# Optimization experiments

Measured on AMD Instinct MI355X. Metric: run time of the kernel, lower is better.

Reference implementation:

```python
import jax, jax.numpy as jnp
import numpy as np

# DH-SFNN: 2 dendritic LIF layers (denri, no tanh, reset-by-subtraction) + leaky readout integrator.
GAMMA = 0.5   # surrogate gradient scale
LENS = 0.5    # surrogate gradient width
VTH = 1.0     # spike threshold
DT = 1.0

@jax.custom_vjp
def spike_fn(x):
    # Heaviside forward, Gaussian surrogate backward (act_fun_adp)
    return (x > 0.0).astype(x.dtype)

def _spike_fwd(x):
    return spike_fn(x), x

def _spike_bwd(x, g):
    sg = GAMMA * jnp.exp(-x * x / (2.0 * LENS * LENS)) / (jnp.sqrt(2.0 * jnp.pi) * LENS)
    return (g * sg,)

spike_fn.defvjp(_spike_fwd, _spike_bwd)

B, T, IN, H, O, K = 256, 250, 700, 256, 20, 4  # batch, time, in_dim, hidden, out_dim, branch
WARMUP = 10


def _branch_mask(rng, out_dim, in_dim, k):
    # Each neuron's k branches see a disjoint random partition of the inputs.
    m = np.zeros((out_dim * k, in_dim), np.float32)
    step = in_dim // k
    for i in range(out_dim):
        perm = rng.permutation(in_dim)
        for j in range(k):
            m[i * k + j, perm[j * step:(j + 1) * step]] = 1.0
    return m


def setup_inputs() -> dict:
    key = jax.random.key(0)
    ks = jax.random.split(key, 12)
    rng = np.random.default_rng(0)
    s1 = 1.0 / np.sqrt(IN)
    s2 = 1.0 / np.sqrt(H)
    # branch-masked dense weights (apply_mask() already baked in)
    W1 = jax.random.uniform(ks[0], (H * K, IN), minval=-s1, maxval=s1) * jnp.asarray(_branch_mask(rng, H, IN, K))
    b1 = jax.random.uniform(ks[1], (H * K,), minval=-s1, maxval=s1)
    tau_n1 = jax.random.uniform(ks[2], (H, K), minval=2.0, maxval=6.0)
    tau_m1 = jax.random.uniform(ks[3], (H,), minval=0.0, maxval=4.0)
    W2 = jax.random.uniform(ks[4], (H * K, H), minval=-s2, maxval=s2) * jnp.asarray(_branch_mask(rng, H, H, K))
    b2 = jax.random.uniform(ks[5], (H * K,), minval=-s2, maxval=s2)
    tau_n2 = jax.random.uniform(ks[6], (H, K), minval=2.0, maxval=6.0)
    tau_m2 = jax.random.uniform(ks[7], (H,), minval=0.0, maxval=4.0)
    Wr = jax.random.uniform(ks[8], (O, H), minval=-s2, maxval=s2)
    br = jax.random.uniform(ks[9], (O,), minval=-s2, maxval=s2)
    tau_mr = jax.random.uniform(ks[10], (O,), minval=0.0, maxval=4.0)
    # sparse binary spike train input (SHD-like)
    x = (jax.random.uniform(ks[11], (B, T, IN)) < 0.1).astype(jnp.float32)
    return dict(x=x, W1=W1, b1=b1, tau_n1=tau_n1, tau_m1=tau_m1,
                W2=W2, b2=b2, tau_n2=tau_n2, tau_m2=tau_m2,
                Wr=Wr, br=br, tau_mr=tau_mr, warmup=WARMUP)


def reference(x, W1, b1, tau_n1, tau_m1, W2, b2, tau_n2, tau_m2, Wr, br, tau_mr, warmup):
    Bb, Tt, _ = x.shape
    beta1 = jax.nn.sigmoid(tau_n1)   # [H,K] dendritic decay
    alpha1 = jax.nn.sigmoid(tau_m1)  # [H]   soma decay
    beta2 = jax.nn.sigmoid(tau_n2)
    alpha2 = jax.nn.sigmoid(tau_m2)
    alphar = jax.nn.sigmoid(tau_mr)  # [O]

    def dense_branch(inp, W, b):
        return (inp @ W.T + b).reshape(inp.shape[0], -1, K)  # [B,H,K]

    def step(carry, xt):
        d1, m1, s1, d2, m2, s2, mr, acc, t = carry
        # layer 1: dendritic filtering then LIF with soft reset
        d1 = beta1 * d1 + (1.0 - beta1) * dense_branch(xt, W1, b1)
        m1 = m1 * alpha1 + (1.0 - alpha1) * DT * d1.sum(-1) - VTH * s1
        s1 = spike_fn(m1 - VTH)
        # layer 2
        d2 = beta2 * d2 + (1.0 - beta2) * dense_branch(s1, W2, b2)
        m2 = m2 * alpha2 + (1.0 - alpha2) * DT * d2.sum(-1) - VTH * s2
        s2 = spike_fn(m2 - VTH)
        # leaky readout integrator
        mr = mr * alphar + (1.0 - alphar) * (s2 @ Wr.T + br)
        acc = acc + jnp.where(t >= warmup, mr, jnp.zeros_like(mr))
        return (d1, m1, s1, d2, m2, s2, mr, acc, t + 1), None

    z = lambda *s: jnp.zeros(s, x.dtype)
    carry0 = (z(Bb, H, K), z(Bb, H), z(Bb, H),
              z(Bb, H, K), z(Bb, H), z(Bb, H),
              z(Bb, O), z(Bb, O), jnp.int32(0))
    carry, _ = jax.lax.scan(step, carry0, jnp.moveaxis(x, 1, 0))
    acc = carry[7]
    return acc / (Tt - warmup)  # readout_mode == 'mean'
```

## Files before the change

### kernel.cpp

```cpp
#include <hip/hip_runtime.h>
#include <hip/hip_bf16.h>

typedef unsigned short us16;
typedef unsigned int u32;
typedef unsigned long long ull;

#define B_   256
#define T_   250
#define IN_  700
#define KP_  704
#define H_   256
#define O_   20
#define HK_  1024
#define NPAIR_ (B_ * T_)
#define LDP_ 40
#define CP_  136
#define CVT_ROWB_ ((NPAIR_ + HK_) / 4)
#define CVT_W2B_  64

typedef __attribute__((ext_vector_type(8))) short short8;
typedef __attribute__((ext_vector_type(4))) float f32x4;

__device__ __forceinline__ float bfbits(unsigned int lo16) {
    union { unsigned int i; float f; } v; v.i = lo16 << 16; return v.f;
}
__device__ __forceinline__ float bflo(unsigned int u) {
    union { unsigned int i; float f; } v; v.i = u << 16; return v.f;
}
__device__ __forceinline__ float bfhi(unsigned int u) {
    union { unsigned int i; float f; } v; v.i = u & 0xffff0000u; return v.f;
}
__device__ __forceinline__ us16 f2bfu(float f) {
    __hip_bfloat16 h = __float2bfloat16(f);
    union { __hip_bfloat16 h; us16 u; } c; c.h = h; return c.u;
}
__device__ __forceinline__ float sigm(float x) { return 1.0f / (1.0f + expf(-x)); }
__device__ __forceinline__ int rfl(int v) { return __builtin_amdgcn_readfirstlane(v); }

__device__ __forceinline__ bool detect_bf16(const us16* __restrict__ taun) {
    int ok = 0;
#pragma unroll
    for (int i = 0; i < 8; i += 2) ok += ((taun[i] >> 8) == 0x40) ? 1 : 0;
    return ok == 4;
}
__device__ __forceinline__ float ldany(const void* __restrict__ p, long i, bool isb) {
    return isb ? bfbits(((const us16*)p)[i]) : ((const float*)p)[i];
}

__device__ __forceinline__ void async_cp16(const us16* g, us16* l) {
    __builtin_amdgcn_global_load_lds(
        (const __attribute__((address_space(1))) u32*)g,
        (__attribute__((address_space(3))) u32*)l, 16, 0, 0);
}

__global__ __launch_bounds__(256) void cvt_rows2(
    const void* __restrict__ xin, const void* __restrict__ w1in,
    const void* __restrict__ w2in,
    us16* __restrict__ xout, us16* __restrict__ w1out,
    us16* __restrict__ w2t,
    const us16* __restrict__ taun) {
    const bool isb = detect_bf16(taun);

    if (blockIdx.x >= CVT_ROWB_) {
        const int base = (blockIdx.x - CVT_ROWB_) * 256 + threadIdx.x;
        for (int e = base; e < H_ * HK_; e += CVT_W2B_ * 256) {
            const int c = e >> 10, n = e & (HK_ - 1);
            w2t[e] = f2bfu(ldany(w2in, (long)n * H_ + c, isb));
        }
        return;
    }

    const int r = blockIdx.x * 4 + (threadIdx.x >> 6);
    const int l = threadIdx.x & 63;
    const void* in; us16* out; long ibase, obase;
    if (r < NPAIR_) {
        in = xin;  out = xout;  ibase = (long)r * IN_; obase = (long)r * KP_;
    } else {
        const int r2 = r - NPAIR_;
        if (r2 >= HK_) return;
        in = w1in; out = w1out; ibase = (long)r2 * IN_; obase = (long)r2 * KP_;
    }
    for (int c = l; c < 88; c += 64) {
        uint4 o;
        if (c < 87) {
            if (isb) {
                uint2 lo = *(const uint2*)((const us16*)in + ibase + 8 * c);
                uint2 hi = *(const uint2*)((const us16*)in + ibase + 8 * c + 4);
                o.x = lo.x; o.y = lo.y; o.z = hi.x; o.w = hi.y;
            } else {
                float4 f0 = *(const float4*)((const float*)in + ibase + 8 * c);
                float4 f1 = *(const float4*)((const float*)in + ibase + 8 * c + 4);
                o.x = (u32)f2bfu(f0.x) | ((u32)f2bfu(f0.y) << 16);
                o.y = (u32)f2bfu(f0.z) | ((u32)f2bfu(f0.w) << 16);
                o.z = (u32)f2bfu(f1.x) | ((u32)f2bfu(f1.y) << 16);
                o.w = (u32)f2bfu(f1.z) | ((u32)f2bfu(f1.w) << 16);
            }
        } else {
            o.z = 0u; o.w = 0u;
            if (isb) {
                uint2 lo = *(const uint2*)((const us16*)in + ibase + 696);
                o.x = lo.x; o.y = lo.y;
            } else {
                float4 f0 = *(const float4*)((const float*)in + ibase + 696);
                o.x = (u32)f2bfu(f0.x) | ((u32)f2bfu(f0.y) << 16);
                o.y = (u32)f2bfu(f0.z) | ((u32)f2bfu(f0.w) << 16);
            }
        }
        *(uint4*)(out + obase + 8 * c) = o;
    }
}

__global__ void transpose_to_bf16(const void* __restrict__ in, us16* __restrict__ out,
                                  int R, int C, const us16* __restrict__ taun) {
    const bool isb = detect_bf16(taun);
    __shared__ us16 tile[32][33];
    int c0 = blockIdx.x * 32, r0 = blockIdx.y * 32;
    int tx = threadIdx.x, ty = threadIdx.y;
#pragma unroll
    for (int j = 0; j < 32; j += 8) {
        int r = r0 + ty + j, c = c0 + tx;
        if (r < R && c < C) tile[ty + j][tx] = f2bfu(ldany(in, (long)r * C + c, isb));
    }
    __syncthreads();
#pragma unroll
    for (int j = 0; j < 32; j += 8) {
        int c = c0 + ty + j, r = r0 + tx;
        if (c < C && r < R) out[(long)c * R + r] = tile[tx][ty + j];
    }
}

__global__ __launch_bounds__(256) void gemm_bf(
    const us16* __restrict__ Xb, const us16* __restrict__ W1b,
    us16* __restrict__ Apre)
{
    __shared__ __align__(16) us16 smem[32768];

    const int L  = blockIdx.x;
    const int mt = (L & 7) + ((L >> 6) << 3);
    const int nt = (L >> 3) & 7;
    if (mt >= NPAIR_ / 128) return;
    const int m0 = mt * 128, n0 = nt * 128;

    const int tid  = threadIdx.x;
    const int lane = tid & 63;
    const int w    = tid >> 6;
    const int wr   = w >> 1, wc = w & 1;
    const int l16  = lane & 15, quad = lane >> 4;

    const int rr    = lane >> 3;
    const int ccsw  = ((lane & 7) ^ rr) * 8;
    const us16* xg[4]; const us16* wg[4];
    int asl[4], bsl[4];
#pragma unroll
    for (int i = 0; i < 4; ++i) {
        const int blkrow = (w * 4 + i) * 8;
        xg[i]  = Xb  + (long)(m0 + blkrow + rr) * KP_ + ccsw;
        wg[i]  = W1b + (long)(n0 + blkrow + rr) * KP_ + ccsw;
        asl[i] = (w * 4 + i) * 512;
        bsl[i] = 8192 + (w * 4 + i) * 512;
    }

    f32x4 acc[4][4];
#pragma unroll
    for (int i = 0; i < 4; ++i)
#pragma unroll
        for (int j = 0; j < 4; ++j) acc[i][j] = (f32x4){0.f, 0.f, 0.f, 0.f};

    const int sw = l16 & 7;
    int aoff0[4], aoff1[4], boff0[4], boff1[4];
#pragma unroll
    for (int i = 0; i < 4; ++i) {
        const int ar = wr * 64 + i * 16 + l16;
        const int br = wc * 64 + i * 16 + l16;
        aoff0[i] = ar * 64 + ((quad ^ sw) << 3);
        aoff1[i] = ar * 64 + (((quad + 4) ^ sw) << 3);
        boff0[i] = 8192 + br * 64 + ((quad ^ sw) << 3);
        boff1[i] = 8192 + br * 64 + (((quad + 4) ^ sw) << 3);
    }

#pragma unroll
    for (int i = 0; i < 4; ++i) async_cp16(xg[i], smem + asl[i]);
#pragma unroll
    for (int i = 0; i < 4; ++i) async_cp16(wg[i], smem + bsl[i]);
    __syncthreads();

    for (int s = 0; s < 11; ++s) {
        const int cur = (s & 1) * 16384;
        const int nxt = 16384 - cur;
        if (s + 1 < 11) {
            const int kb = (s + 1) * 64;
#pragma unroll
            for (int i = 0; i < 4; ++i) async_cp16(xg[i] + kb, smem + nxt + asl[i]);
#pragma unroll
            for (int i = 0; i < 4; ++i) async_cp16(wg[i] + kb, smem + nxt + bsl[i]);
        }

        short8 af[4][2], bfv[4][2];
#pragma unroll
        for (int i = 0; i < 4; ++i) {
            af[i][0]  = *(const short8*)(smem + cur + aoff0[i]);
            af[i][1]  = *(const short8*)(smem + cur + aoff1[i]);
            bfv[i][0] = *(const short8*)(smem + cur + boff0[i]);
            bfv[i][1] = *(const short8*)(smem + cur + boff1[i]);
        }
#pragma unroll
        for (int h = 0; h < 2; ++h)
#pragma unroll
            for (int i = 0; i < 4; ++i)
#pragma unroll
                for (int j = 0; j < 4; ++j)
                    acc[i][j] = __builtin_amdgcn_mfma_f32_16x16x32_bf16(
                        af[i][h], bfv[j][h], acc[i][j], 0, 0, 0);

        __syncthreads();
    }

#pragma unroll
    for (int i = 0; i < 4; ++i)
#pragma unroll
        for (int j = 0; j < 4; ++j)
#pragma unroll
            for (int r = 0; r < 4; ++r)
                smem[(wr * 64 + i * 16 + quad * 4 + r) * CP_ +
                     (wc * 64 + j * 16 + l16)] = f2bfu(acc[i][j][r]);
    __syncthreads();
    {
        const int c8 = (lane & 15) * 8;
#pragma unroll
        for (int r2 = 0; r2 < 8; ++r2) {
            const int row = w * 32 + r2 * 4 + (lane >> 4);
            const uint4 v = *(const uint4*)(smem + row * CP_ + c8);
            *(uint4*)(Apre + (long)(m0 + row) * HK_ + n0 + c8) = v;
        }
    }
}

__device__ void wave_recur(
    const us16* __restrict__ Apre,
    const void* __restrict__ b1,  const void* __restrict__ tau_n1,
    const void* __restrict__ tau_m1,
    const void* __restrict__ b2,  const void* __restrict__ tau_n2,
    const void* __restrict__ tau_m2,
    const void* __restrict__ Wr,  const void* __restrict__ br,
    const void* __restrict__ tau_mr,
    const us16* __restrict__ W2T,
    int wu, bool isb, int b, int lane,
    void* __restrict__ out)
{
    float be1[16], cb1[16], be2[16], cb2[16], d1[16], d2[16];
#pragma unroll
    for (int e = 0; e < 16; ++e) {
        const long gi = (long)lane * 16 + e;
        const float t1 = sigm(ldany(tau_n1, gi, isb));
        be1[e] = t1; cb1[e] = (1.f - t1) * ldany(b1, gi, isb);
        const float t2 = sigm(ldany(tau_n2, gi, isb));
        be2[e] = t2; cb2[e] = (1.f - t2) * ldany(b2, gi, isb);
        d1[e] = 0.f; d2[e] = 0.f;
    }
    float al1[4], al2[4], m1[4], s1[4], m2[4], s2[4];
#pragma unroll
    for (int j = 0; j < 4; ++j) {
        al1[j] = sigm(ldany(tau_m1, lane * 4 + j, isb));
        al2[j] = sigm(ldany(tau_m2, lane * 4 + j, isb));
        m1[j] = 0.f; s1[j] = 0.f; m2[j] = 0.f; s2[j] = 0.f;
    }
    float alr = 0.f, brv = 0.f;
    if (lane < O_) { alr = sigm(ldany(tau_mr, lane, isb)); brv = ldany(br, lane, isb); }
    float mrv = 0.f, accO = 0.f;

    const us16* ap = Apre + (long)b * T_ * HK_ + lane * 16;

    auto wstep = [&](int t, uint4 lo, uint4 hi) {
        float a[16];
        a[0]=bflo(lo.x);  a[1]=bfhi(lo.x);  a[2]=bflo(lo.y);  a[3]=bfhi(lo.y);
        a[4]=bflo(lo.z);  a[5]=bfhi(lo.z);  a[6]=bflo(lo.w);  a[7]=bfhi(lo.w);
        a[8]=bflo(hi.x);  a[9]=bfhi(hi.x);  a[10]=bflo(hi.y); a[11]=bfhi(hi.y);
        a[12]=bflo(hi.z); a[13]=bfhi(hi.z); a[14]=bflo(hi.w); a[15]=bfhi(hi.w);
#pragma unroll
        for (int e = 0; e < 16; ++e)
            d1[e] = be1[e] * d1[e] + cb1[e] + (1.f - be1[e]) * a[e];
        unsigned long long bal1[4];
#pragma unroll
        for (int j = 0; j < 4; ++j) {
            const float s = (d1[j*4+0] + d1[j*4+1]) + (d1[j*4+2] + d1[j*4+3]);
            m1[j] = m1[j] * al1[j] + (1.f - al1[j]) * s - s1[j];
            s1[j] = (m1[j] > 1.0f) ? 1.f : 0.f;
            bal1[j] = __ballot(s1[j] > 0.f);
        }
        if ((bal1[0] | bal1[1] | bal1[2] | bal1[3]) != 0ull) {
            float g[16];
#pragma unroll
            for (int e = 0; e < 16; ++e) g[e] = 0.f;
            for (int j2 = 0; j2 < 4; ++j2) {
                unsigned long long mm = bal1[j2];
                while (mm) {
                    const int i = __ffsll(mm) - 1; mm &= mm - 1;
                    const us16* wv = W2T + ((long)(i * 4 + j2) << 10) + lane * 16;
                    const uint4 wl = *(const uint4*)wv;
                    const uint4 wh = *(const uint4*)(wv + 8);
                    g[0]+=bflo(wl.x);  g[1]+=bfhi(wl.x);  g[2]+=bflo(wl.y);  g[3]+=bfhi(wl.y);
                    g[4]+=bflo(wl.z);  g[5]+=bfhi(wl.z);  g[6]+=bflo(wl.w);  g[7]+=bfhi(wl.w);
                    g[8]+=bflo(wh.x);  g[9]+=bfhi(wh.x);  g[10]+=bflo(wh.y); g[11]+=bfhi(wh.y);
                    g[12]+=bflo(wh.z); g[13]+=bfhi(wh.z); g[14]+=bflo(wh.w); g[15]+=bfhi(wh.w);
                }
            }
#pragma unroll
            for (int e = 0; e < 16; ++e)
                d2[e] = be2[e] * d2[e] + cb2[e] + (1.f - be2[e]) * g[e];
        } else {
#pragma unroll
            for (int e = 0; e < 16; ++e)
                d2[e] = be2[e] * d2[e] + cb2[e];
        }
        unsigned long long bal2[4];
#pragma unroll
        for (int j = 0; j < 4; ++j) {
            const float s = (d2[j*4+0] + d2[j*4+1]) + (d2[j*4+2] + d2[j*4+3]);
            m2[j] = m2[j] * al2[j] + (1.f - al2[j]) * s - s2[j];
            s2[j] = (m2[j] > 1.0f) ? 1.f : 0.f;
            bal2[j] = __ballot(s2[j] > 0.f);
        }
        if (lane < O_) {
            float sum = brv;
            if ((bal2[0] | bal2[1] | bal2[2] | bal2[3]) != 0ull) {
                for (int j2 = 0; j2 < 4; ++j2) {
                    unsigned long long mm = bal2[j2];
                    while (mm) {
                        const int i = __ffsll(mm) - 1; mm &= mm - 1;
                        sum += ldany(Wr, (long)lane * H_ + (i * 4 + j2), isb);
                    }
                }
            }
            mrv = alr * mrv + (1.f - alr) * sum;
            if (t >= wu) accO += mrv;
        }
    };

    uint4 q0a = *(const uint4*)(ap);
    uint4 q0b = *(const uint4*)(ap + 8);
    uint4 q1a = *(const uint4*)(ap + HK_);
    uint4 q1b = *(const uint4*)(ap + HK_ + 8);
    uint4 q2a = *(const uint4*)(ap + 2 * HK_);
    uint4 q2b = *(const uint4*)(ap + 2 * HK_ + 8);
    uint4 q3a = *(const uint4*)(ap + 3 * HK_);
    uint4 q3b = *(const uint4*)(ap + 3 * HK_ + 8);

    int t = 0;
    for (int it = 0; it < 62; ++it) {
        wstep(t + 0, q0a, q0b);
        q0a = *(const uint4*)(ap + (long)(t + 4) * HK_);
        q0b = *(const uint4*)(ap + (long)(t + 4) * HK_ + 8);
        wstep(t + 1, q1a, q1b);
        if (t + 5 < T_) {
            q1a = *(const uint4*)(ap + (long)(t + 5) * HK_);
            q1b = *(const uint4*)(ap + (long)(t + 5) * HK_ + 8);
        }
        wstep(t + 2, q2a, q2b);
        if (t + 6 < T_) {
            q2a = *(const uint4*)(ap + (long)(t + 6) * HK_);
            q2b = *(const uint4*)(ap + (long)(t + 6) * HK_ + 8);
        }
        wstep(t + 3, q3a, q3b);
        if (t + 7 < T_) {
            q3a = *(const uint4*)(ap + (long)(t + 7) * HK_);
            q3b = *(const uint4*)(ap + (long)(t + 7) * HK_ + 8);
        }
        t += 4;
    }
    wstep(248, q0a, q0b);
    wstep(249, q1a, q1b);

    if (lane < O_) {
        const float res = accO / (float)(T_ - wu);
        if (isb) ((us16*)out)[b * O_ + lane] = f2bfu(res);
        else     ((float*)out)[b * O_ + lane] = res;
    }
}

__global__ __launch_bounds__(320) void l1_fused(
    const us16* __restrict__ Apre,
    const void* __restrict__ b1,  const void* __restrict__ tau_n1,
    const void* __restrict__ tau_m1,
    const void* __restrict__ b2,  const void* __restrict__ tau_n2,
    const void* __restrict__ tau_m2,
    const void* __restrict__ Wr,  const void* __restrict__ br,
    const void* __restrict__ tau_mr,
    const us16* __restrict__ W2T,
    const int* __restrict__ warmup_p,
    void* __restrict__ out)
{
    __shared__ ull wany[4];

    const int tid  = threadIdx.x;
    const int lane = tid & 63;
    const int w    = tid >> 6;
    const int b    = blockIdx.x;
    const bool isb = detect_bf16((const us16*)tau_n1);
    const int wu   = *warmup_p;

    if (w == 4) {
        float be2[16], cb2[16], d2[16], al2[4], m2[4], s2[4];
#pragma unroll
        for (int e = 0; e < 16; ++e) {
            const long gi = (long)lane * 16 + e;
            const float t2 = sigm(ldany(tau_n2, gi, isb));
            be2[e] = t2; cb2[e] = (1.f - t2) * ldany(b2, gi, isb);
            d2[e] = 0.f;
        }
#pragma unroll
        for (int j = 0; j < 4; ++j) {
            al2[j] = sigm(ldany(tau_m2, lane * 4 + j, isb));
            m2[j] = 0.f; s2[j] = 0.f;
        }
        float alr = 0.f, brv = 0.f;
        if (lane < O_) { alr = sigm(ldany(tau_mr, lane, isb)); brv = ldany(br, lane, isb); }
        float mrv = 0.f, accO = 0.f;

        for (int t = 0; t < T_; ++t) {
#pragma unroll
            for (int e = 0; e < 16; ++e)
                d2[e] = be2[e] * d2[e] + cb2[e];
            unsigned long long bal2[4];
#pragma unroll
            for (int j = 0; j < 4; ++j) {
                const float s2s = (d2[j*4+0] + d2[j*4+1]) + (d2[j*4+2] + d2[j*4+3]);
                m2[j] = m2[j] * al2[j] + (1.f - al2[j]) * s2s - s2[j];
                s2[j] = (m2[j] > 1.0f) ? 1.f : 0.f;
                bal2[j] = __ballot(s2[j] > 0.f);
            }
            if (lane < O_) {
                float sum = brv;
                if ((bal2[0] | bal2[1] | bal2[2] | bal2[3]) != 0ull) {
                    for (int j2 = 0; j2 < 4; ++j2) {
                        unsigned long long mm = bal2[j2];
                        while (mm) {
                            const int i = __ffsll(mm) - 1; mm &= mm - 1;
                            sum += ldany(Wr, (long)lane * H_ + (i * 4 + j2), isb);
                        }
                    }
                }
                mrv = alr * mrv + (1.f - alr) * sum;
                if (t >= wu) accO += mrv;
            }
        }
        __syncthreads();
        const ull flag = wany[0] | wany[1] | wany[2] | wany[3];
        if (flag == 0ull && lane < O_) {
            const float res = accO / (float)(T_ - wu);
            if (isb) ((us16*)out)[b * O_ + lane] = f2bfu(res);
            else     ((float*)out)[b * O_ + lane] = res;
        }
        return;
    }

    float be1[4], cb1[4], ce1[4], d1[4];
#pragma unroll
    for (int k = 0; k < 4; ++k) {
        const long gi = 4L * tid + k;
        const float t1 = sigm(ldany(tau_n1, gi, isb));
        be1[k] = t1; ce1[k] = 1.f - t1; cb1[k] = ce1[k] * ldany(b1, gi, isb);
        d1[k] = 0.f;
    }
    const float al1 = sigm(ldany(tau_m1, tid, isb)), cal1 = 1.f - al1;
    float m1 = 0.f, s1f = 0.f;
    int any = 0;

    const us16* ap = Apre + (long)b * T_ * HK_ + 4 * tid;

    uint2 q0 = *(const uint2*)(ap);
    uint2 q1 = *(const uint2*)(ap + HK_);
    uint2 q2 = *(const uint2*)(ap + 2 * HK_);
    uint2 q3 = *(const uint2*)(ap + 3 * HK_);
    uint2 q4 = *(const uint2*)(ap + 4 * HK_);
    uint2 q5 = *(const uint2*)(ap + 5 * HK_);
    uint2 q6 = *(const uint2*)(ap + 6 * HK_);
    uint2 q7 = *(const uint2*)(ap + 7 * HK_);

    auto body = [&](int t, uint2& q) {
        const float a0 = bflo(q.x), a1 = bfhi(q.x), a2 = bflo(q.y), a3 = bfhi(q.y);
        if (t + 8 < T_) q = *(const uint2*)(ap + (long)(t + 8) * HK_);
        d1[0] = be1[0] * d1[0] + cb1[0] + ce1[0] * a0;
        d1[1] = be1[1] * d1[1] + cb1[1] + ce1[1] * a1;
        d1[2] = be1[2] * d1[2] + cb1[2] + ce1[2] * a2;
        d1[3] = be1[3] * d1[3] + cb1[3] + ce1[3] * a3;
        const float s = (d1[0] + d1[1]) + (d1[2] + d1[3]);
        m1 = m1 * al1 + cal1 * s - s1f;
        const int sp = (m1 > 1.0f) ? 1 : 0;
        s1f = sp ? 1.f : 0.f;
        any |= sp;
    };

    int t = 0;
    for (int it = 0; it < 31; ++it) {
        body(t + 0, q0); body(t + 1, q1); body(t + 2, q2); body(t + 3, q3);
        body(t + 4, q4); body(t + 5, q5); body(t + 6, q6); body(t + 7, q7);
        t += 8;
    }
    body(248, q0);
    body(249, q1);

    const ull bm = __ballot(any != 0);
    if (lane == 0) wany[w] = bm;
    __syncthreads();
    const ull flag = wany[0] | wany[1] | wany[2] | wany[3];

    if (w == 0 && flag != 0ull) {
        wave_recur(Apre, b1, tau_n1, tau_m1, b2, tau_n2, tau_m2,
                   Wr, br, tau_mr, W2T, wu, isb, b, lane, out);
    }
}

#define GA_LOAD(S, AV, BV) do {                                               \
    const int k0_ = (S) * 32 + half16;                                        \
    if (k0_ + 16 <= IN_) {                                                    \
        if (isb) {                                                            \
            const us16* pa_ = (const us16*)X  + arow + k0_;                   \
            const us16* pb_ = (const us16*)W1 + brow + k0_;                   \
            uint2 a0_ = *(const uint2*)pa_,        a1_ = *(const uint2*)(pa_ + 4);  \
            uint2 a2_ = *(const uint2*)(pa_ + 8),  a3_ = *(const uint2*)(pa_ + 12); \
            uint2 b0_ = *(const uint2*)pb_,        b1_ = *(const uint2*)(pb_ + 4);  \
            uint2 b2_ = *(const uint2*)(pb_ + 8),  b3_ = *(const uint2*)(pb_ + 12); \
            AV[0]=a0_.x; AV[1]=a0_.y; AV[2]=a1_.x; AV[3]=a1_.y;               \
            AV[4]=a2_.x; AV[5]=a2_.y; AV[6]=a3_.x; AV[7]=a3_.y;               \
            BV[0]=b0_.x; BV[1]=b0_.y; BV[2]=b1_.x; BV[3]=b1_.y;               \
            BV[4]=b2_.x; BV[5]=b2_.y; BV[6]=b3_.x; BV[7]=b3_.y;               \
        } else {                                                              \
            const float* pa_ = (const float*)X  + arow + k0_;                 \
            const float* pb_ = (const float*)W1 + brow + k0_;                 \
            float4 fa0_ = *(const float4*)pa_,        fa1_ = *(const float4*)(pa_ + 4);  \
            float4 fa2_ = *(const float4*)(pa_ + 8),  fa3_ = *(const float4*)(pa_ + 12); \
            float4 fb0_ = *(const float4*)pb_,        fb1_ = *(const float4*)(pb_ + 4);  \
            float4 fb2_ = *(const float4*)(pb_ + 8),  fb3_ = *(const float4*)(pb_ + 12); \
            AV[0] = (unsigned)f2bfu(fa0_.x) | ((unsigned)f2bfu(fa0_.y) << 16); \
            AV[1] = (unsigned)f2bfu(fa0_.z) | ((unsigned)f2bfu(fa0_.w) << 16); \
            AV[2] = (unsigned)f2bfu(fa1_.x) | ((unsigned)f2bfu(fa1_.y) << 16); \
            AV[3] = (unsigned)f2bfu(fa1_.z) | ((unsigned)f2bfu(fa1_.w) << 16); \
            AV[4] = (unsigned)f2bfu(fa2_.x) | ((unsigned)f2bfu(fa2_.y) << 16); \
            AV[5] = (unsigned)f2bfu(fa2_.z) | ((unsigned)f2bfu(fa2_.w) << 16); \
            AV[6] = (unsigned)f2bfu(fa3_.x) | ((unsigned)f2bfu(fa3_.y) << 16); \
            AV[7] = (unsigned)f2bfu(fa3_.z) | ((unsigned)f2bfu(fa3_.w) << 16); \
            BV[0] = (unsigned)f2bfu(fb0_.x) | ((unsigned)f2bfu(fb0_.y) << 16); \
            BV[1] = (unsigned)f2bfu(fb0_.z) | ((unsigned)f2bfu(fb0_.w) << 16); \
            BV[2] = (unsigned)f2bfu(fb1_.x) | ((unsigned)f2bfu(fb1_.y) << 16); \
            BV[3] = (unsigned)f2bfu(fb1_.z) | ((unsigned)f2bfu(fb1_.w) << 16); \
            BV[4] = (unsigned)f2bfu(fb2_.x) | ((unsigned)f2bfu(fb2_.y) << 16); \
            BV[5] = (unsigned)f2bfu(fb2_.z) | ((unsigned)f2bfu(fb2_.w) << 16); \
            BV[6] = (unsigned)f2bfu(fb3_.x) | ((unsigned)f2bfu(fb3_.y) << 16); \
            BV[7] = (unsigned)f2bfu(fb3_.z) | ((unsigned)f2bfu(fb3_.w) << 16); \
        }                                                                     \
    } else {                                                                  \
        _Pragma("unroll")                                                     \
        for (int e_ = 0; e_ < 8; ++e_) { AV[e_] = 0u; BV[e_] = 0u; }          \
        _Pragma("unroll")                                                     \
        for (int e_ = 0; e_ < 16; ++e_) {                                     \
            int k_ = k0_ + e_;                                                \
            if (k_ < IN_) {                                                   \
                unsigned va_ = (unsigned)f2bfu(ldany(X,  arow + k_, isb));    \
                unsigned vb_ = (unsigned)f2bfu(ldany(W1, brow + k_, isb));    \
                AV[e_ >> 1] |= va_ << ((e_ & 1) * 16);                        \
                BV[e_ >> 1] |= vb_ << ((e_ & 1) * 16);                        \
            }                                                                 \
        }                                                                     \
    }                                                                         \
} while (0)

#define GA_STORE(AV, BV) do {                                                 \
    uint4 u0_; u0_.x = AV[0]; u0_.y = AV[1]; u0_.z = AV[2]; u0_.w = AV[3];    \
    uint4 u1_; u1_.x = AV[4]; u1_.y = AV[5]; u1_.z = AV[6]; u1_.w = AV[7];    \
    uint4 v0_; v0_.x = BV[0]; v0_.y = BV[1]; v0_.z = BV[2]; v0_.w = BV[3];    \
    uint4 v1_; v1_.x = BV[4]; v1_.y = BV[5]; v1_.z = BV[6]; v1_.w = BV[7];    \
    *(uint4*)asw       = u0_; *(uint4*)(asw + 8) = u1_;                       \
    *(uint4*)bsw       = v0_; *(uint4*)(bsw + 8) = v1_;                       \
} while (0)

#define GA_MFMA() do {                                                        \
    short8 af_[4], bf_[4];                                                    \
    _Pragma("unroll")                                                         \
    for (int i_ = 0; i_ < 4; ++i_) af_[i_] = *(const short8*)(As + aoff[i_]); \
    _Pragma("unroll")                                                         \
    for (int j_ = 0; j_ < 4; ++j_) bf_[j_] = *(const short8*)(Bs + boff[j_]); \
    _Pragma("unroll")                                                         \
    for (int i_ = 0; i_ < 4; ++i_)                                            \
        _Pragma("unroll")                                                     \
        for (int j_ = 0; j_ < 4; ++j_)                                        \
            acc[i_][j_] = __builtin_amdgcn_mfma_f32_16x16x32_bf16(            \
                af_[i_], bf_[j_], acc[i_][j_], 0, 0, 0);                      \
} while (0)

__global__ __launch_bounds__(256) void gemm_apre(
    const void* __restrict__ X, const void* __restrict__ W1,
    const us16* __restrict__ taun, us16* __restrict__ Apre)
{
    const bool isb = detect_bf16(taun);
    __shared__ __align__(16) us16 As[128 * LDP_];
    __shared__ __align__(16) us16 Bs[128 * LDP_];

    const int L  = blockIdx.x;
    const int mt = (L & 7) + ((L >> 6) << 3);
    const int nt = (L >> 3) & 7;
    if (mt >= NPAIR_ / 128) return;
    const int m0 = mt * 128, n0 = nt * 128;

    const int tid  = threadIdx.x;
    const int lane = tid & 63;
    const int w    = tid >> 6;
    const int wr   = w >> 1, wc = w & 1;
    const int l16  = lane & 15, quad = lane >> 4;
    const int ra   = tid >> 1;
    const int half16 = (tid & 1) * 16;

    f32x4 acc[4][4];
#pragma unroll
    for (int i = 0; i < 4; ++i)
#pragma unroll
        for (int j = 0; j < 4; ++j) acc[i][j] = (f32x4){0.f, 0.f, 0.f, 0.f};

    int aoff[4], boff[4];
#pragma unroll
    for (int i = 0; i < 4; ++i) {
        aoff[i] = (wr * 64 + i * 16 + l16) * LDP_ + quad * 8;
        boff[i] = (wc * 64 + i * 16 + l16) * LDP_ + quad * 8;
    }

    const long arow = (long)(m0 + ra) * IN_;
    const long brow = (long)(n0 + ra) * IN_;
    us16* asw = As + ra * LDP_ + half16;
    us16* bsw = Bs + ra * LDP_ + half16;

    unsigned av0[8], bv0[8], av1[8], bv1[8];
    GA_LOAD(0, av0, bv0);

    for (int ss = 0; ss < 11; ++ss) {
        __syncthreads();
        GA_STORE(av0, bv0);
        __syncthreads();
        GA_LOAD(2 * ss + 1, av1, bv1);
        GA_MFMA();
        __syncthreads();
        GA_STORE(av1, bv1);
        __syncthreads();
        if (ss < 10) GA_LOAD(2 * ss + 2, av0, bv0);
        GA_MFMA();
    }

#pragma unroll
    for (int i = 0; i < 4; ++i) {
#pragma unroll
        for (int j = 0; j < 4; ++j) {
            const int gm = m0 + wr * 64 + i * 16 + quad * 4;
            const int gn = n0 + wc * 64 + j * 16 + l16;
            us16* op = Apre + (long)gm * HK_ + gn;
#pragma unroll
            for (int r = 0; r < 4; ++r)
                op[(long)r * HK_] = f2bfu(acc[i][j][r]);
        }
    }
}

__global__ __launch_bounds__(64) void dhsfnn_wave(
    const us16* __restrict__ Apre,
    const void* __restrict__ b1,  const void* __restrict__ tau_n1,
    const void* __restrict__ tau_m1,
    const void* __restrict__ b2,  const void* __restrict__ tau_n2,
    const void* __restrict__ tau_m2,
    const void* __restrict__ Wr,  const void* __restrict__ br,
    const void* __restrict__ tau_mr,
    const us16* __restrict__ W2T,
    const int* __restrict__ warmup_p,
    void* __restrict__ out)
{
    const int lane = threadIdx.x;
    const int b    = blockIdx.x;
    const bool isb = detect_bf16((const us16*)tau_n1);
    const int wu   = *warmup_p;
    wave_recur(Apre, b1, tau_n1, tau_m1, b2, tau_n2, tau_m2,
               Wr, br, tau_mr, W2T, wu, isb, b, lane, out);
}

__global__ __launch_bounds__(256) void dhsfnn_fb(
    const void* __restrict__ x,  const void* __restrict__ W1,
    const void* __restrict__ b1, const void* __restrict__ tau_n1,
    const void* __restrict__ tau_m1,
    const void* __restrict__ W2, const void* __restrict__ b2,
    const void* __restrict__ tau_n2, const void* __restrict__ tau_m2,
    const void* __restrict__ Wr, const void* __restrict__ br,
    const void* __restrict__ tau_mr,
    const int* __restrict__ warmup_p,
    void* __restrict__ out)
{
    __shared__ us16 list1[1024];
    __shared__ us16 list2[256];
    __shared__ us16 list3[256];
    __shared__ int n1s, n2s, n3s;

    const int tid = threadIdx.x;
    const int b   = blockIdx.x;
    const int h   = tid;
    const bool isb = detect_bf16((const us16*)tau_n1);
    const int wu  = *warmup_p;

    const float be1_0 = sigm(ldany(tau_n1, 4 * h + 0, isb));
    const float be1_1 = sigm(ldany(tau_n1, 4 * h + 1, isb));
    const float be1_2 = sigm(ldany(tau_n1, 4 * h + 2, isb));
    const float be1_3 = sigm(ldany(tau_n1, 4 * h + 3, isb));
    const float bi1_0 = ldany(b1, 4 * h + 0, isb), bi1_1 = ldany(b1, 4 * h + 1, isb);
    const float bi1_2 = ldany(b1, 4 * h + 2, isb), bi1_3 = ldany(b1, 4 * h + 3, isb);
    const float al1 = sigm(ldany(tau_m1, h, isb));
    const float be2_0 = sigm(ldany(tau_n2, 4 * h + 0, isb));
    const float be2_1 = sigm(ldany(tau_n2, 4 * h + 1, isb));
    const float be2_2 = sigm(ldany(tau_n2, 4 * h + 2, isb));
    const float be2_3 = sigm(ldany(tau_n2, 4 * h + 3, isb));
    const float bi2_0 = ldany(b2, 4 * h + 0, isb), bi2_1 = ldany(b2, 4 * h + 1, isb);
    const float bi2_2 = ldany(b2, 4 * h + 2, isb), bi2_3 = ldany(b2, 4 * h + 3, isb);
    const float al2 = sigm(ldany(tau_m2, h, isb));
    float alr = 0.f, brv = 0.f;
    if (h < O_) { alr = sigm(ldany(tau_mr, h, isb)); brv = ldany(br, h, isb); }

    float d1_0 = 0.f, d1_1 = 0.f, d1_2 = 0.f, d1_3 = 0.f, m1v = 0.f, s1f = 0.f;
    float d2_0 = 0.f, d2_1 = 0.f, d2_2 = 0.f, d2_3 = 0.f, m2v = 0.f, s2f = 0.f;
    float mrv = 0.f, accO = 0.f;

    const long xbase = (long)b * T_ * IN_;
    float xv0 = ldany(x, xbase + tid, isb);
    float xv1 = ldany(x, xbase + tid + 256, isb);
    float xv2 = (tid + 512 < IN_) ? ldany(x, xbase + tid + 512, isb) : 0.f;

    for (int t = 0; t < T_; ++t) {
        const bool p0 = xv0 != 0.f, p1 = xv1 != 0.f, p2 = xv2 != 0.f;
        if (t + 1 < T_) {
            const long nbx = xbase + (long)(t + 1) * IN_;
            xv0 = ldany(x, nbx + tid, isb);
            xv1 = ldany(x, nbx + tid + 256, isb);
            xv2 = (tid + 512 < IN_) ? ldany(x, nbx + tid + 512, isb) : 0.f;
        }
        __syncthreads();
        if (tid == 0) { n1s = 0; n2s = 0; n3s = 0; }
        __syncthreads();
        if (p0) { int p = atomicAdd(&n1s, 1); list1[p & 1023] = (us16)tid; }
        if (p1) { int p = atomicAdd(&n1s, 1); list1[p & 1023] = (us16)(tid + 256); }
        if (p2) { int p = atomicAdd(&n1s, 1); list1[p & 1023] = (us16)(tid + 512); }
        __syncthreads();
        int n1 = n1s; n1 = (n1 < 1024) ? n1 : 1024;

        float a0 = 0.f, a1 = 0.f, a2 = 0.f, a3 = 0.f;
#pragma unroll 2
        for (int idx = 0; idx < n1; ++idx) {
            int i = rfl((int)list1[idx]);
            i = (i < IN_) ? i : (IN_ - 1);
            long r = (long)(h * 4) * IN_ + i;
            a0 += ldany(W1, r, isb);
            a1 += ldany(W1, r + IN_, isb);
            a2 += ldany(W1, r + 2 * IN_, isb);
            a3 += ldany(W1, r + 3 * IN_, isb);
        }
        d1_0 = be1_0 * d1_0 + (1.f - be1_0) * (bi1_0 + a0);
        d1_1 = be1_1 * d1_1 + (1.f - be1_1) * (bi1_1 + a1);
        d1_2 = be1_2 * d1_2 + (1.f - be1_2) * (bi1_2 + a2);
        d1_3 = be1_3 * d1_3 + (1.f - be1_3) * (bi1_3 + a3);
        m1v = m1v * al1 + (1.f - al1) * (d1_0 + d1_1 + d1_2 + d1_3) - s1f;
        s1f = (m1v > 1.0f) ? 1.f : 0.f;

        if (s1f > 0.f) { int p = atomicAdd(&n2s, 1); list2[p & 255] = (us16)tid; }
        __syncthreads();
        int n2 = n2s; n2 = (n2 < 256) ? n2 : 256;

        a0 = 0.f; a1 = 0.f; a2 = 0.f; a3 = 0.f;
#pragma unroll 2
        for (int idx = 0; idx < n2; ++idx) {
            int i = rfl((int)list2[idx]);
            i = (i < H_) ? i : (H_ - 1);
            long r = (long)(h * 4) * H_ + i;
            a0 += ldany(W2, r, isb);
            a1 += ldany(W2, r + H_, isb);
            a2 += ldany(W2, r + 2 * H_, isb);
            a3 += ldany(W2, r + 3 * H_, isb);
        }
        d2_0 = be2_0 * d2_0 + (1.f - be2_0) * (bi2_0 + a0);
        d2_1 = be2_1 * d2_1 + (1.f - be2_1) * (bi2_1 + a1);
        d2_2 = be2_2 * d2_2 + (1.f - be2_2) * (bi2_2 + a2);
        d2_3 = be2_3 * d2_3 + (1.f - be2_3) * (bi2_3 + a3);
        m2v = m2v * al2 + (1.f - al2) * (d2_0 + d2_1 + d2_2 + d2_3) - s2f;
        s2f = (m2v > 1.0f) ? 1.f : 0.f;

        if (s2f > 0.f) { int p = atomicAdd(&n3s, 1); list3[p & 255] = (us16)tid; }
        __syncthreads();
        int n3 = n3s; n3 = (n3 < 256) ? n3 : 256;

        if (h < O_) {
            float sum = brv;
            for (int idx = 0; idx < n3; ++idx) {
                int j = (int)list3[idx];
                j = (j < H_) ? j : (H_ - 1);
                sum += ldany(Wr, (long)h * H_ + j, isb);
            }
            mrv = alr * mrv + (1.f - alr) * sum;
            if (t >= wu) accO += mrv;
        }
    }
    if (h < O_) {
        float res = accO / (float)(T_ - wu);
        if (isb) ((us16*)out)[b * O_ + h] = f2bfu(res);
        else     ((float*)out)[b * O_ + h] = res;
    }
}

extern "C" void kernel_launch(void* const* d_in, const int* in_sizes, int n_in,
                              void* d_out, int out_size, void* d_ws, size_t ws_size,
                              hipStream_t stream) {
    const void* x      = d_in[0];
    const void* W1     = d_in[1];
    const void* b1     = d_in[2];
    const void* tau_n1 = d_in[3];
    const void* tau_m1 = d_in[4];
    const void* W2     = d_in[5];
    const void* b2     = d_in[6];
    const void* tau_n2 = d_in[7];
    const void* tau_m2 = d_in[8];
    const void* Wr     = d_in[9];
    const void* br     = d_in[10];
    const void* tau_mr = d_in[11];
    const int*  warmup = (const int*)d_in[12];

    const size_t w2t_bytes  = (size_t)H_ * HK_ * 2;
    const size_t xbf_bytes  = (size_t)NPAIR_ * KP_ * 2;
    const size_t w1b_bytes  = (size_t)HK_ * KP_ * 2;
    const size_t apre_bytes = (size_t)NPAIR_ * HK_ * 2;

    const bool tier0 = (d_ws != nullptr &&
                        ws_size >= w2t_bytes + xbf_bytes + w1b_bytes + apre_bytes);
    const bool tier1 = (d_ws != nullptr && ws_size >= w2t_bytes + apre_bytes);

    dim3 blk(32, 8);
    if (tier0) {
        us16* W2T  = (us16*)d_ws;
        us16* Xbf  = (us16*)((char*)d_ws + w2t_bytes);
        us16* W1bf = (us16*)((char*)d_ws + w2t_bytes + xbf_bytes);
        us16* Apre = (us16*)((char*)d_ws + w2t_bytes + xbf_bytes + w1b_bytes);

        cvt_rows2<<<CVT_ROWB_ + CVT_W2B_, 256, 0, stream>>>(
            x, W1, W2, Xbf, W1bf, W2T, (const us16*)tau_n1);
        gemm_bf<<<4096, 256, 0, stream>>>(Xbf, W1bf, Apre);
        l1_fused<<<B_, 320, 0, stream>>>(
            Apre, b1, tau_n1, tau_m1, b2, tau_n2, tau_m2,
            Wr, br, tau_mr, W2T, warmup, d_out);
    } else if (tier1) {
        us16* W2T  = (us16*)d_ws;
        us16* Apre = (us16*)((char*)d_ws + w2t_bytes);
        transpose_to_bf16<<<dim3((H_ + 31) / 32, (HK_ + 31) / 32), blk, 0, stream>>>(
            W2, W2T, HK_, H_, (const us16*)tau_n1);
        gemm_apre<<<4096, 256, 0, stream>>>(x, W1, (const us16*)tau_n1, Apre);
        dhsfnn_wave<<<B_, 64, 0, stream>>>(
            Apre, b1, tau_n1, tau_m1, b2, tau_n2, tau_m2,
            Wr, br, tau_mr, W2T, warmup, d_out);
    } else {
        dhsfnn_fb<<<B_, 256, 0, stream>>>(x, W1, b1, tau_n1, tau_m1,
                                          W2, b2, tau_n2, tau_m2,
                                          Wr, br, tau_mr, warmup, d_out);
    }
}
```

Baseline: 408.3 us.

## Rewrite layer-1 GEMM with 256x256 tiles, 512 threads, triple-buffered async loads

After: 464.1 us. 13.6% more time.

```diff
diff --git a/kernel.cpp b/kernel.cpp
--- a/kernel.cpp
+++ b/kernel.cpp
@@ -14,7 +14,6 @@
 #define HK_  1024
 #define NPAIR_ (B_ * T_)
 #define LDP_ 40
-#define CP_  136
 #define CVT_ROWB_ ((NPAIR_ + HK_) / 4)
 #define CVT_W2B_  64
 
@@ -129,109 +128,113 @@
     }
 }
 
-__global__ __launch_bounds__(256) void gemm_bf(
+__global__ __launch_bounds__(512, 2) void gemm8(
     const us16* __restrict__ Xb, const us16* __restrict__ W1b,
     us16* __restrict__ Apre)
 {
-    __shared__ __align__(16) us16 smem[32768];
-
-    const int L  = blockIdx.x;
-    const int mt = (L & 7) + ((L >> 6) << 3);
-    const int nt = (L >> 3) & 7;
-    if (mt >= NPAIR_ / 128) return;
-    const int m0 = mt * 128, n0 = nt * 128;
+    __shared__ __align__(16) us16 smem[49152];
+
+    const int bid = blockIdx.x;
+    const int mt  = bid >> 2, nt = bid & 3;
+    const int m0  = mt * 256, n0 = nt * 256;
 
     const int tid  = threadIdx.x;
     const int lane = tid & 63;
     const int w    = tid >> 6;
-    const int wr   = w >> 1, wc = w & 1;
+    const int wr   = w >> 2, wc = w & 3;
     const int l16  = lane & 15, quad = lane >> 4;
 
-    const int rr    = lane >> 3;
-    const int ccsw  = ((lane & 7) ^ rr) * 8;
-    const us16* xg[4]; const us16* wg[4];
-    int asl[4], bsl[4];
-#pragma unroll
-    for (int i = 0; i < 4; ++i) {
-        const int blkrow = (w * 4 + i) * 8;
-        xg[i]  = Xb  + (long)(m0 + blkrow + rr) * KP_ + ccsw;
-        wg[i]  = W1b + (long)(n0 + blkrow + rr) * KP_ + ccsw;
-        asl[i] = (w * 4 + i) * 512;
-        bsl[i] = 8192 + (w * 4 + i) * 512;
-    }
-
-    f32x4 acc[4][4];
-#pragma unroll
-    for (int i = 0; i < 4; ++i)
-#pragma unroll
-        for (int j = 0; j < 4; ++j) acc[i][j] = (f32x4){0.f, 0.f, 0.f, 0.f};
-
-    const int sw = l16 & 7;
-    int aoff0[4], aoff1[4], boff0[4], boff1[4];
-#pragma unroll
-    for (int i = 0; i < 4; ++i) {
-        const int ar = wr * 64 + i * 16 + l16;
-        const int br = wc * 64 + i * 16 + l16;
-        aoff0[i] = ar * 64 + ((quad ^ sw) << 3);
-        aoff1[i] = ar * 64 + (((quad + 4) ^ sw) << 3);
-        boff0[i] = 8192 + br * 64 + ((quad ^ sw) << 3);
-        boff1[i] = 8192 + br * 64 + (((quad + 4) ^ sw) << 3);
-    }
-
-#pragma unroll
-    for (int i = 0; i < 4; ++i) async_cp16(xg[i], smem + asl[i]);
-#pragma unroll
-    for (int i = 0; i < 4; ++i) async_cp16(wg[i], smem + bsl[i]);
-    __syncthreads();
-
-    for (int s = 0; s < 11; ++s) {
-        const int cur = (s & 1) * 16384;
-        const int nxt = 16384 - cur;
-        if (s + 1 < 11) {
-            const int kb = (s + 1) * 64;
-#pragma unroll
-            for (int i = 0; i < 4; ++i) async_cp16(xg[i] + kb, smem + nxt + asl[i]);
-#pragma unroll
-            for (int i = 0; i < 4; ++i) async_cp16(wg[i] + kb, smem + nxt + bsl[i]);
-        }
-
-        short8 af[4][2], bfv[4][2];
-#pragma unroll
-        for (int i = 0; i < 4; ++i) {
-            af[i][0]  = *(const short8*)(smem + cur + aoff0[i]);
-            af[i][1]  = *(const short8*)(smem + cur + aoff1[i]);
-            bfv[i][0] = *(const short8*)(smem + cur + boff0[i]);
-            bfv[i][1] = *(const short8*)(smem + cur + boff1[i]);
-        }
-#pragma unroll
-        for (int h = 0; h < 2; ++h)
-#pragma unroll
-            for (int i = 0; i < 4; ++i)
-#pragma unroll
-                for (int j = 0; j < 4; ++j)
-                    acc[i][j] = __builtin_amdgcn_mfma_f32_16x16x32_bf16(
-                        af[i][h], bfv[j][h], acc[i][j], 0, 0, 0);
-
-        __syncthreads();
-    }
-
-#pragma unroll
-    for (int i = 0; i < 4; ++i)
-#pragma unroll
-        for (int j = 0; j < 4; ++j)
-#pragma unroll
-            for (int r = 0; r < 4; ++r)
-                smem[(wr * 64 + i * 16 + quad * 4 + r) * CP_ +
-                     (wc * 64 + j * 16 + l16)] = f2bfu(acc[i][j][r]);
-    __syncthreads();
-    {
-        const int c8 = (lane & 15) * 8;
-#pragma unroll
-        for (int r2 = 0; r2 < 8; ++r2) {
-            const int row = w * 32 + r2 * 4 + (lane >> 4);
-            const uint4 v = *(const uint4*)(smem + row * CP_ + c8);
-            *(uint4*)(Apre + (long)(m0 + row) * HK_ + n0 + c8) = v;
-        }
+    const int srow = tid >> 2;
+    const int sskc = (((tid & 3) ^ (srow & 3)) << 3);
+    const us16* xg = Xb  + (long)(m0 + srow) * KP_ + sskc;
+    const us16* wg = W1b + (long)(n0 + srow) * KP_ + sskc;
+    const int sl = tid * 8;
+
+    auto stage = [&](int kt, int boff) {
+        const int kb = kt * 32;
+        async_cp16(xg + kb,                   smem + boff + sl);
+        async_cp16(xg + (long)128 * KP_ + kb, smem + boff + 4096 + sl);
+        async_cp16(wg + kb,                   smem + boff + 8192 + sl);
+        async_cp16(wg + (long)128 * KP_ + kb, smem + boff + 12288 + sl);
+    };
+
+    const int ksw = ((quad ^ (l16 & 3)) << 3);
+    int aoff[8], boffr[4];
+#pragma unroll
+    for (int mf = 0; mf < 8; ++mf)
+        aoff[mf] = (wr * 128 + mf * 16 + l16) * 32 + ksw;
+#pragma unroll
+    for (int nf = 0; nf < 4; ++nf)
+        boffr[nf] = 8192 + (wc * 64 + nf * 16 + l16) * 32 + ksw;
+
+    f32x4 acc[8][4];
+#pragma unroll
+    for (int mf = 0; mf < 8; ++mf)
+#pragma unroll
+        for (int nf = 0; nf < 4; ++nf) acc[mf][nf] = (f32x4){0.f, 0.f, 0.f, 0.f};
+
+    stage(0, 0);
+    stage(1, 16384);
+    asm volatile("s_waitcnt vmcnt(4)" ::: "memory");
+    __builtin_amdgcn_s_barrier();
+
+    int bcur = 0;
+    for (int kt = 0; kt < 22; ++kt) {
+        if (kt <= 19) {
+            int b2 = bcur + 32768;
+            if (b2 >= 49152) b2 -= 49152;
+            stage(kt + 2, b2);
+        }
+
+        short8 af[8], bf[4];
+#pragma unroll
+        for (int mf = 0; mf < 8; ++mf)
+            af[mf] = *(const short8*)(smem + bcur + aoff[mf]);
+#pragma unroll
+        for (int nf = 0; nf < 4; ++nf)
+            bf[nf] = *(const short8*)(smem + bcur + boffr[nf]);
+
+        __builtin_amdgcn_s_setprio(1);
+#pragma unroll
+        for (int mf = 0; mf < 8; ++mf)
+#pragma unroll
+            for (int nf = 0; nf < 4; ++nf)
+                acc[mf][nf] = __builtin_amdgcn_mfma_f32_16x16x32_bf16(
+                    af[mf], bf[nf], acc[mf][nf], 0, 0, 0);
+        __builtin_amdgcn_s_setprio(0);
+
+        __builtin_amdgcn_sched_barrier(0);
+        if (kt <= 19)
+            asm volatile("s_waitcnt vmcnt(4) lgkmcnt(0)\n\ts_barrier" ::: "memory");
+        else
+            asm volatile("s_waitcnt vmcnt(0) lgkmcnt(0)\n\ts_barrier" ::: "memory");
+
+        bcur += 16384; if (bcur >= 49152) bcur = 0;
+    }
+
+    const int erow = tid >> 2;
+    const int ecol = (tid & 3) * 64;
+#pragma unroll
+    for (int half = 0; half < 2; ++half) {
+        if (wr == half) {
+#pragma unroll
+            for (int mf = 0; mf < 8; ++mf)
+#pragma unroll
+                for (int nf = 0; nf < 4; ++nf)
+#pragma unroll
+                    for (int r = 0; r < 4; ++r)
+                        smem[(mf * 16 + quad * 4 + r) * 256 +
+                             wc * 64 + nf * 16 + l16] = f2bfu(acc[mf][nf][r]);
+        }
+        __syncthreads();
+        {
+            us16* gp = Apre + (long)(m0 + half * 128 + erow) * HK_ + n0 + ecol;
+            const us16* sp = smem + erow * 256 + ecol;
+#pragma unroll
+            for (int j = 0; j < 8; ++j)
+                *(uint4*)(gp + j * 8) = *(const uint4*)(sp + j * 8);
+        }
+        __syncthreads();
     }
 }
 
@@ -839,7 +842,7 @@
 
         cvt_rows2<<<CVT_ROWB_ + CVT_W2B_, 256, 0, stream>>>(
             x, W1, W2, Xbf, W1bf, W2T, (const us16*)tau_n1);
-        gemm_bf<<<4096, 256, 0, stream>>>(Xbf, W1bf, Apre);
+        gemm8<<<1000, 512, 0, stream>>>(Xbf, W1bf, Apre);
         l1_fused<<<B_, 320, 0, stream>>>(
             Apre, b1, tau_n1, tau_m1, b2, tau_n2, tau_m2,
             Wr, br, tau_mr, W2T, warmup, d_out);
```

## Triple-buffer input-projection GEMM with 32-wide K tiles and finer waits

Applied to the files above, without the earlier changes.

Result: slower. 427.1 us (+4.6%).

```diff
diff --git a/kernel.cpp b/kernel.cpp
--- a/kernel.cpp
+++ b/kernel.cpp
@@ -129,11 +129,11 @@
     }
 }
 
-__global__ __launch_bounds__(256) void gemm_bf(
+__global__ __launch_bounds__(256, 3) void gemm_bf32(
     const us16* __restrict__ Xb, const us16* __restrict__ W1b,
     us16* __restrict__ Apre)
 {
-    __shared__ __align__(16) us16 smem[32768];
+    __shared__ __align__(16) us16 smem[24576];
 
     const int L  = blockIdx.x;
     const int mt = (L & 7) + ((L >> 6) << 3);
@@ -147,17 +147,19 @@
     const int wr   = w >> 1, wc = w & 1;
     const int l16  = lane & 15, quad = lane >> 4;
 
-    const int rr    = lane >> 3;
-    const int ccsw  = ((lane & 7) ^ rr) * 8;
-    const us16* xg[4]; const us16* wg[4];
-    int asl[4], bsl[4];
+    const int ksrc = (((tid & 3) ^ ((tid >> 3) & 3)) << 3);
+    const us16* xg0 = Xb  + (long)(m0 +      (tid >> 2)) * KP_ + ksrc;
+    const us16* xg1 = Xb  + (long)(m0 + 64 + (tid >> 2)) * KP_ + ksrc;
+    const us16* wg0 = W1b + (long)(n0 +      (tid >> 2)) * KP_ + ksrc;
+    const us16* wg1 = W1b + (long)(n0 + 64 + (tid >> 2)) * KP_ + ksrc;
+    const int sl = tid * 8;
+
+    const int csw = ((quad ^ ((l16 >> 1) & 3)) << 3);
+    int aoff[4], boff[4];
 #pragma unroll
     for (int i = 0; i < 4; ++i) {
-        const int blkrow = (w * 4 + i) * 8;
-        xg[i]  = Xb  + (long)(m0 + blkrow + rr) * KP_ + ccsw;
-        wg[i]  = W1b + (long)(n0 + blkrow + rr) * KP_ + ccsw;
-        asl[i] = (w * 4 + i) * 512;
-        bsl[i] = 8192 + (w * 4 + i) * 512;
+        aoff[i] = (wr * 64 + i * 16 + l16) * 32 + csw;
+        boff[i] = 4096 + (wc * 64 + i * 16 + l16) * 32 + csw;
     }
 
     f32x4 acc[4][4];
@@ -166,53 +168,49 @@
 #pragma unroll
         for (int j = 0; j < 4; ++j) acc[i][j] = (f32x4){0.f, 0.f, 0.f, 0.f};
 
-    const int sw = l16 & 7;
-    int aoff0[4], aoff1[4], boff0[4], boff1[4];
-#pragma unroll
-    for (int i = 0; i < 4; ++i) {
-        const int ar = wr * 64 + i * 16 + l16;
-        const int br = wc * 64 + i * 16 + l16;
-        aoff0[i] = ar * 64 + ((quad ^ sw) << 3);
-        aoff1[i] = ar * 64 + (((quad + 4) ^ sw) << 3);
-        boff0[i] = 8192 + br * 64 + ((quad ^ sw) << 3);
-        boff1[i] = 8192 + br * 64 + (((quad + 4) ^ sw) << 3);
-    }
-
-#pragma unroll
-    for (int i = 0; i < 4; ++i) async_cp16(xg[i], smem + asl[i]);
-#pragma unroll
-    for (int i = 0; i < 4; ++i) async_cp16(wg[i], smem + bsl[i]);
-    __syncthreads();
-
-    for (int s = 0; s < 11; ++s) {
-        const int cur = (s & 1) * 16384;
-        const int nxt = 16384 - cur;
-        if (s + 1 < 11) {
-            const int kb = (s + 1) * 64;
-#pragma unroll
-            for (int i = 0; i < 4; ++i) async_cp16(xg[i] + kb, smem + nxt + asl[i]);
-#pragma unroll
-            for (int i = 0; i < 4; ++i) async_cp16(wg[i] + kb, smem + nxt + bsl[i]);
-        }
-
-        short8 af[4][2], bfv[4][2];
+    auto stage = [&](int kt, int be) {
+        const int kb = kt * 32;
+        async_cp16(xg0 + kb, smem + be + sl);
+        async_cp16(xg1 + kb, smem + be + 2048 + sl);
+        async_cp16(wg0 + kb, smem + be + 4096 + sl);
+        async_cp16(wg1 + kb, smem + be + 6144 + sl);
+    };
+
+    stage(0, 0);
+    stage(1, 8192);
+    asm volatile("s_waitcnt vmcnt(4)" ::: "memory");
+    __builtin_amdgcn_s_barrier();
+
+    int bcur = 0;
+    for (int kt = 0; kt < 22; ++kt) {
+        if (kt <= 19) {
+            int b2 = bcur + 16384;
+            if (b2 >= 24576) b2 -= 24576;
+            stage(kt + 2, b2);
+        }
+
+        short8 af[4], bfv[4];
 #pragma unroll
         for (int i = 0; i < 4; ++i) {
-            af[i][0]  = *(const short8*)(smem + cur + aoff0[i]);
-            af[i][1]  = *(const short8*)(smem + cur + aoff1[i]);
-            bfv[i][0] = *(const short8*)(smem + cur + boff0[i]);
-            bfv[i][1] = *(const short8*)(smem + cur + boff1[i]);
-        }
-#pragma unroll
-        for (int h = 0; h < 2; ++h)
-#pragma unroll
-            for (int i = 0; i < 4; ++i)
-#pragma unroll
-                for (int j = 0; j < 4; ++j)
-                    acc[i][j] = __builtin_amdgcn_mfma_f32_16x16x32_bf16(
-                        af[i][h], bfv[j][h], acc[i][j], 0, 0, 0);
-
-        __syncthreads();
+            af[i]  = *(const short8*)(smem + bcur + aoff[i]);
+            bfv[i] = *(const short8*)(smem + bcur + boff[i]);
+        }
+        __builtin_amdgcn_s_setprio(1);
+#pragma unroll
+        for (int i = 0; i < 4; ++i)
+#pragma unroll
+            for (int j = 0; j < 4; ++j)
+                acc[i][j] = __builtin_amdgcn_mfma_f32_16x16x32_bf16(
+                    af[i], bfv[j], acc[i][j], 0, 0, 0);
+        __builtin_amdgcn_s_setprio(0);
+
+        __builtin_amdgcn_sched_barrier(0);
+        if (kt <= 19)
+            asm volatile("s_waitcnt vmcnt(4) lgkmcnt(0)\n\ts_barrier" ::: "memory");
+        else
+            asm volatile("s_waitcnt vmcnt(0) lgkmcnt(0)\n\ts_barrier" ::: "memory");
+
+        bcur += 8192; if (bcur >= 24576) bcur = 0;
     }
 
 #pragma unroll
@@ -839,7 +837,7 @@
 
         cvt_rows2<<<CVT_ROWB_ + CVT_W2B_, 256, 0, stream>>>(
             x, W1, W2, Xbf, W1bf, W2T, (const us16*)tau_n1);
-        gemm_bf<<<4096, 256, 0, stream>>>(Xbf, W1bf, Apre);
+        gemm_bf32<<<4096, 256, 0, stream>>>(Xbf, W1bf, Apre);
         l1_fused<<<B_, 320, 0, stream>>>(
             Apre, b1, tau_n1, tau_m1, b2, tau_n2, tau_m2,
             Wr, br, tau_mr, W2T, warmup, d_out);
```
